# Kernel tuning notes

Measured on AMD Instinct MI355X. Metric: run time of the kernel, lower is better.

## Reference

```python
import jax, jax.numpy as jnp
import numpy as np

N_EMBD = 1024
HEAD_SIZE = 64  # n_embd // n_head = 1024 // 16


def setup_inputs() -> dict:
    key = jax.random.key(0)
    ks = jax.random.split(key, 7)
    B, T, C, H = 4, 2048, N_EMBD, HEAD_SIZE
    s = 1.0 / np.sqrt(C)
    return {
        "x": jax.random.normal(ks[0], (B, T, C), dtype=jnp.float32),
        "Wq": jax.random.normal(ks[1], (C, H), dtype=jnp.float32) * s,
        "bq": jax.random.normal(ks[2], (H,), dtype=jnp.float32) * 0.01,
        "Wk": jax.random.normal(ks[3], (C, H), dtype=jnp.float32) * s,
        "bk": jax.random.normal(ks[4], (H,), dtype=jnp.float32) * 0.01,
        "Wv": jax.random.normal(ks[5], (C, H), dtype=jnp.float32) * s,
        "bv": jax.random.normal(ks[6], (H,), dtype=jnp.float32) * 0.01,
    }


def reference(x, Wq, bq, Wk, bk, Wv, bv):
    # x: [B, T, C]
    B, T, C = x.shape
    q = x @ Wq + bq  # [B, T, H]
    k = x @ Wk + bk  # [B, T, H]
    v = x @ Wv + bv  # [B, T, H]
    # NOTE: original module does NOT scale by 1/sqrt(head_size)
    wei = jnp.einsum("bth,bsh->bts", q, k)  # [B, T, T]
    causal = jnp.tril(jnp.ones((T, T), dtype=bool))
    wei = jnp.where(causal, wei, -jnp.inf)
    wei = jax.nn.softmax(wei, axis=-1)
    out = jnp.einsum("bts,bsh->bth", wei, v)  # [B, T, H]
    return out
```

## Files before the change

kernel.cpp:

```cpp
#include <hip/hip_runtime.h>

typedef float f32x4 __attribute__((ext_vector_type(4)));
typedef short s16x4 __attribute__((ext_vector_type(4)));
typedef short s16x8 __attribute__((ext_vector_type(8)));

#define LOG2E 1.4426950408889634f

__device__ __forceinline__ short f2bf(float f) {
  unsigned u = __float_as_uint(f);
  unsigned r = (u + 0x7fffu + ((u >> 16) & 1u)) >> 16;
  return (short)r;
}
__device__ __forceinline__ float bf2f(short s) {
  return __uint_as_float(((unsigned)(unsigned short)s) << 16);
}
__device__ __forceinline__ unsigned cvt_pk_bf16(float a, float b) {
  unsigned r;
  asm("v_cvt_pk_bf16_f32 %0, %1, %2" : "=v"(r) : "v"(a), "v"(b));
  return r;
}

__device__ __forceinline__ f32x4 mfma16(s16x4 a, s16x4 b, f32x4 c) {
  return __builtin_amdgcn_mfma_f32_16x16x16bf16_1k(a, b, c, 0, 0, 0);
}
__device__ __forceinline__ f32x4 mfma32(s16x8 a, s16x8 b, f32x4 c) {
  return __builtin_amdgcn_mfma_f32_16x16x32_bf16(a, b, c, 0, 0, 0);
}

__device__ __forceinline__ void gl_lds16(const void* gp, void* sp) {
  __builtin_amdgcn_global_load_lds(
      (__attribute__((address_space(1))) void*)const_cast<void*>(gp),
      (__attribute__((address_space(3))) void*)sp, 16, 0, 0);
}

__global__ __launch_bounds__(256) void prep_w(
    const float* __restrict__ Wq, const float* __restrict__ Wk, const float* __restrict__ Wv,
    short* __restrict__ wt_hi, short* __restrict__ wt_lo) {
  int idx = blockIdx.x * 256 + threadIdx.x;
  int n = idx >> 10;
  int c = idx & 1023;
  const float* W = (n < 64) ? Wq : ((n < 128) ? Wk : Wv);
  float v = W[c * 64 + (n & 63)];
  short hi = f2bf(v);
  short lo = f2bf(v - bf2f(hi));
  wt_hi[idx] = hi;
  wt_lo[idx] = lo;
}

__global__ __launch_bounds__(512, 2) void proj_qkv(
    const float* __restrict__ x,
    const short* __restrict__ wt_hi, const short* __restrict__ wt_lo,
    const float* __restrict__ bq, const float* __restrict__ bk, const float* __restrict__ bv,
    short* __restrict__ q_hi, short* __restrict__ q_lo,
    short* __restrict__ k_hi, short* __restrict__ k_lo,
    short* __restrict__ v_t) {
  const int tid = threadIdx.x;
  const int lane = tid & 63;
  const int wv = tid >> 6;
  const int col = lane & 15;
  const int g = lane >> 4;
  const int mg = wv >> 2;
  const int ng = wv & 3;
  const int tokbase = blockIdx.x * 32;

  __shared__ short lds[5][12288];

  const int wsl = ((lane & 3) ^ ((lane >> 3) & 3)) * 8;
  const short* s0 = wt_hi + (size_t)(16 * wv + (lane >> 2)) * 1024 + wsl;
  const int d0 = wv * 512;
  const int c1 = wv + 8;
  const short* s1 = (c1 < 12 ? wt_hi + (size_t)(16 * c1 + (lane >> 2)) * 1024
                             : wt_lo + (size_t)(16 * (c1 - 12) + (lane >> 2)) * 1024) + wsl;
  const int d1 = (c1 < 12) ? c1 * 512 : 6144 + (c1 - 12) * 512;
  const int c2 = wv + 16;
  const bool isx = (c2 >= 20);
  const short* s2 = isx
      ? (const short*)(x + (size_t)(tokbase + 8 * (c2 - 20) + (lane >> 3)) * 1024 +
                       ((lane & 7) ^ (lane >> 3)) * 4)
      : wt_lo + (size_t)(16 * (c2 - 12) + (lane >> 2)) * 1024 + wsl;
  const int d2 = isx ? 10240 + (c2 - 20) * 512 : 6144 + (c2 - 12) * 512;
  const int st2 = isx ? 64 : 32;

#define STAGE(BP, S) do { \
    gl_lds16(s0 + (S) * 32, (BP) + d0); \
    gl_lds16(s1 + (S) * 32, (BP) + d1); \
    gl_lds16(s2 + (S) * st2, (BP) + d2); \
  } while (0)

#define PIPE_WAIT(N) do { \
    asm volatile("s_waitcnt vmcnt(" #N ")" ::: "memory"); \
    __builtin_amdgcn_s_barrier(); \
    __builtin_amdgcn_sched_barrier(0); \
  } while (0)
#define PIPE_END do { \
    asm volatile("s_waitcnt lgkmcnt(0)" ::: "memory"); \
    __builtin_amdgcn_sched_barrier(0); \
    __builtin_amdgcn_s_barrier(); \
  } while (0)

  const int arow = mg * 16 + col;
  const int xq0 = ((2 * g) ^ (arow & 7)) << 2;
  const int xq1 = ((2 * g + 1) ^ (arow & 7)) << 2;
  const int rq = ng * 16 + col;
  const int ws = (g ^ ((rq >> 1) & 3)) << 3;

  f32x4 accQ = {0,0,0,0}, accK = {0,0,0,0}, accV = {0,0,0,0};

  typedef union { unsigned u[4]; s16x8 v8; } pk8;

#define COMPUTE(BP) do { \
    const short* bp_ = (BP); \
    const float* xb_ = (const float*)(bp_ + 10240); \
    f32x4 x0_ = *(const f32x4*)(xb_ + arow * 32 + xq0); \
    f32x4 x1_ = *(const f32x4*)(xb_ + arow * 32 + xq1); \
    pk8 xh_, xl_; \
    xh_.u[0] = cvt_pk_bf16(x0_[0], x0_[1]); \
    xh_.u[1] = cvt_pk_bf16(x0_[2], x0_[3]); \
    xh_.u[2] = cvt_pk_bf16(x1_[0], x1_[1]); \
    xh_.u[3] = cvt_pk_bf16(x1_[2], x1_[3]); \
    xl_.u[0] = cvt_pk_bf16(x0_[0] - __uint_as_float(xh_.u[0] << 16), \
                           x0_[1] - __uint_as_float(xh_.u[0] & 0xffff0000u)); \
    xl_.u[1] = cvt_pk_bf16(x0_[2] - __uint_as_float(xh_.u[1] << 16), \
                           x0_[3] - __uint_as_float(xh_.u[1] & 0xffff0000u)); \
    xl_.u[2] = cvt_pk_bf16(x1_[0] - __uint_as_float(xh_.u[2] << 16), \
                           x1_[1] - __uint_as_float(xh_.u[2] & 0xffff0000u)); \
    xl_.u[3] = cvt_pk_bf16(x1_[2] - __uint_as_float(xh_.u[3] << 16), \
                           x1_[3] - __uint_as_float(xh_.u[3] & 0xffff0000u)); \
    s16x8 qh_ = *(const s16x8*)(bp_ + rq * 32 + ws); \
    s16x8 kh_ = *(const s16x8*)(bp_ + (64 + rq) * 32 + ws); \
    s16x8 vh_ = *(const s16x8*)(bp_ + (128 + rq) * 32 + ws); \
    s16x8 ql_ = *(const s16x8*)(bp_ + 6144 + rq * 32 + ws); \
    s16x8 kl_ = *(const s16x8*)(bp_ + 6144 + (64 + rq) * 32 + ws); \
    accQ = mfma32(xh_.v8, qh_, accQ); \
    accK = mfma32(xh_.v8, kh_, accK); \
    accV = mfma32(xh_.v8, vh_, accV); \
    accQ = mfma32(xl_.v8, qh_, accQ); \
    accK = mfma32(xl_.v8, kh_, accK); \
    accQ = mfma32(xh_.v8, ql_, accQ); \
    accK = mfma32(xh_.v8, kl_, accK); \
  } while (0)

  short* cA = &lds[0][0];
  short* cB = &lds[1][0];
  short* cC = &lds[2][0];
  short* cD = &lds[3][0];
  short* cE = &lds[4][0];

  STAGE(cA, 0); STAGE(cB, 1); STAGE(cC, 2); STAGE(cD, 3);

#pragma unroll 1
  for (int b = 0; b < 28; ++b) {
    STAGE(cE, b + 4);
    PIPE_WAIT(12);
    COMPUTE(cA);
    PIPE_END;
    short* t = cA; cA = cB; cB = cC; cC = cD; cD = cE; cE = t;
  }
  PIPE_WAIT(9); COMPUTE(cA); PIPE_END;
  PIPE_WAIT(6); COMPUTE(cB); PIPE_END;
  PIPE_WAIT(3); COMPUTE(cC); PIPE_END;
  PIPE_WAIT(0); COMPUTE(cD);

  {
    const int hQ = ng * 16 + col;
    const float biasq = bq[hQ];
    const float biask = bk[hQ];
    const float biasv = bv[hQ];
#pragma unroll
    for (int r = 0; r < 4; ++r) {
      const int tok = tokbase + mg * 16 + 4 * g + r;
      float fq = accQ[r] + biasq;
      short qh = f2bf(fq);
      q_hi[(size_t)tok * 64 + hQ] = qh;
      q_lo[(size_t)tok * 64 + hQ] = f2bf(fq - bf2f(qh));
      float fk = accK[r] + biask;
      short kh = f2bf(fk);
      k_hi[(size_t)tok * 64 + hQ] = kh;
      k_lo[(size_t)tok * 64 + hQ] = f2bf(fk - bf2f(kh));
      const int bb = tok >> 11;
      const int tl = tok & 2047;
      v_t[((size_t)bb * 64 + hQ) * 2048 + tl] = f2bf(accV[r] + biasv);
    }
  }
#undef STAGE
#undef PIPE_WAIT
#undef PIPE_END
#undef COMPUTE
}

__global__ __launch_bounds__(512, 2) void attn(
    const short* __restrict__ q_hi, const short* __restrict__ q_lo,
    const short* __restrict__ k_hi, const short* __restrict__ k_lo,
    const short* __restrict__ v_t,
    float* __restrict__ pm, float* __restrict__ pl, float* __restrict__ pO) {
  const int tid = threadIdx.x;
  const int lane = tid & 63;
  const int w = tid >> 6;
  const int col = lane & 15;
  const int g = lane >> 4;
  const int bid = blockIdx.x;
  const int p = bid & 7;
  const int b = (bid >> 3) & 3;
  const int s = bid >> 5;
  if (s > p) return;

  __shared__ short lds[3][12288];

  const int qlo = 256 * p + 32 * w;
  const int kb0 = 256 * s;

  const short* qbh = q_hi + (size_t)(b * 2048 + qlo + col) * 64 + g * 8;
  const short* qbl = q_lo + (size_t)(b * 2048 + qlo + col) * 64 + g * 8;
  s16x8 qh0a = *(const s16x8*)(qbh);
  s16x8 qh1a = *(const s16x8*)(qbh + 32);
  s16x8 ql0a = *(const s16x8*)(qbl);
  s16x8 ql1a = *(const s16x8*)(qbl + 32);
  s16x8 qh0b = *(const s16x8*)(qbh + 16 * 64);
  s16x8 qh1b = *(const s16x8*)(qbh + 16 * 64 + 32);
  s16x8 ql0b = *(const s16x8*)(qbl + 16 * 64);
  s16x8 ql1b = *(const s16x8*)(qbl + 16 * 64 + 32);
  asm volatile("s_waitcnt vmcnt(0)" ::: "memory");
  __builtin_amdgcn_sched_barrier(0);

  f32x4 oA0 = {0,0,0,0}, oA1 = {0,0,0,0}, oA2 = {0,0,0,0}, oA3 = {0,0,0,0};
  f32x4 oB0 = {0,0,0,0}, oB1 = {0,0,0,0}, oB2 = {0,0,0,0}, oB3 = {0,0,0,0};
  float mA = -3.0e38f, lA = 0.0f, mB = -3.0e38f, lB = 0.0f;
  const f32x4 NEGV = {-3.0e38f, -3.0e38f, -3.0e38f, -3.0e38f};

#define STAGE(BP, J) do { \
    const int kbs_ = kb0 + 64 * (J); \
    const int r_ = 8 * w + (lane >> 3); \
    const int lc_ = (lane & 7) ^ (lane >> 3); \
    gl_lds16(k_hi + (size_t)(b * 2048 + kbs_ + r_) * 64 + lc_ * 8, (BP) + 8 * w * 64); \
    gl_lds16(k_lo + (size_t)(b * 2048 + kbs_ + r_) * 64 + lc_ * 8, (BP) + 4096 + 8 * w * 64); \
    gl_lds16(v_t + ((size_t)b * 64 + r_) * 2048 + kbs_ + lc_ * 8, (BP) + 8192 + 8 * w * 64); \
  } while (0)

#define PIPE_WAIT(N) do { \
    asm volatile("s_waitcnt vmcnt(" #N ")" ::: "memory"); \
    __builtin_amdgcn_s_barrier(); \
    __builtin_amdgcn_sched_barrier(0); \
  } while (0)
#define PIPE_END do { \
    asm volatile("s_waitcnt lgkmcnt(0)" ::: "memory"); \
    __builtin_amdgcn_sched_barrier(0); \
    __builtin_amdgcn_s_barrier(); \
  } while (0)

#define QK_U(U) do { \
    const int kg0_ = kb_ + 16 * U; \
    if (kg0_ <= qlo + 31) { \
      const short* kr_ = bp_ + (16 * U + col) * 64; \
      const int cx_ = col & 7; \
      s16x8 kh0_ = *(const s16x8*)(kr_ + ((g ^ cx_) << 3)); \
      s16x8 kh1_ = *(const s16x8*)(kr_ + (((4 + g) ^ cx_) << 3)); \
      s16x8 kl0_ = *(const s16x8*)(kr_ + 4096 + ((g ^ cx_) << 3)); \
      s16x8 kl1_ = *(const s16x8*)(kr_ + 4096 + (((4 + g) ^ cx_) << 3)); \
      if (kg0_ <= qlo + 15) { \
        f32x4 u1_ = {0,0,0,0}, u2_ = {0,0,0,0}; \
        u1_ = mfma32(kh0_, qh0a, u1_); u1_ = mfma32(kh1_, qh1a, u1_); \
        u2_ = mfma32(kh0_, ql0a, u2_); u2_ = mfma32(kh1_, ql1a, u2_); \
        u2_ = mfma32(kl0_, qh0a, u2_); u2_ = mfma32(kl1_, qh1a, u2_); \
        scA##U = u1_ + u2_; \
        if (kg0_ == qlo) { \
          _Pragma("unroll") for (int i = 0; i < 4; ++i) \
            if (4 * g + i > col) scA##U[i] = -3.0e38f; \
        } \
      } \
      { \
        f32x4 u1_ = {0,0,0,0}, u2_ = {0,0,0,0}; \
        u1_ = mfma32(kh0_, qh0b, u1_); u1_ = mfma32(kh1_, qh1b, u1_); \
        u2_ = mfma32(kh0_, ql0b, u2_); u2_ = mfma32(kh1_, ql1b, u2_); \
        u2_ = mfma32(kl0_, qh0b, u2_); u2_ = mfma32(kl1_, qh1b, u2_); \
        scB##U = u1_ + u2_; \
        if (kg0_ == qlo + 16) { \
          _Pragma("unroll") for (int i = 0; i < 4; ++i) \
            if (4 * g + i > col) scB##U[i] = -3.0e38f; \
        } \
      } \
    } \
  } while (0)

#define SMAX4(v) fmaxf(fmaxf((v)[0], (v)[1]), fmaxf((v)[2], (v)[3]))

#define SOFTMAX_X(s0v, s1v, s2v, s3v, mX, lX, o0X, o1X, o2X, o3X, p0X, p1X, p2X, p3X) do { \
    float mx_ = fmaxf(fmaxf(SMAX4(s0v), SMAX4(s1v)), fmaxf(SMAX4(s2v), SMAX4(s3v))); \
    mx_ = fmaxf(mx_, __shfl_xor(mx_, 16)); \
    mx_ = fmaxf(mx_, __shfl_xor(mx_, 32)); \
    const float mn_ = fmaxf(mX, mx_); \
    const float rs_ = __builtin_amdgcn_exp2f((mX - mn_) * LOG2E); \
    float ls_ = 0.f; \
    _Pragma("unroll") for (int i = 0; i < 4; ++i) { \
      float e0_ = __builtin_amdgcn_exp2f((s0v[i] - mn_) * LOG2E); \
      float e1_ = __builtin_amdgcn_exp2f((s1v[i] - mn_) * LOG2E); \
      float e2_ = __builtin_amdgcn_exp2f((s2v[i] - mn_) * LOG2E); \
      float e3_ = __builtin_amdgcn_exp2f((s3v[i] - mn_) * LOG2E); \
      p0X[i] = f2bf(e0_); p1X[i] = f2bf(e1_); p2X[i] = f2bf(e2_); p3X[i] = f2bf(e3_); \
      ls_ += e0_ + e1_ + e2_ + e3_; \
    } \
    lX = lX * rs_ + ls_; \
    o0X *= rs_; o1X *= rs_; o2X *= rs_; o3X *= rs_; \
    mX = mn_; \
  } while (0)

#define PV_U(U) do { \
    const int kg0_ = kb_ + 16 * U; \
    if (kg0_ <= qlo + 31) { \
      const int cx_ = col & 7; \
      const short* vr_ = bp_ + 8192 + col * 64 + ((g & 1) << 2) + \
                         (((2 * U + (g >> 1)) ^ cx_) << 3); \
      s16x4 v0_ = *(const s16x4*)(vr_); \
      s16x4 v1_ = *(const s16x4*)(vr_ + 1024); \
      s16x4 v2_ = *(const s16x4*)(vr_ + 2048); \
      s16x4 v3_ = *(const s16x4*)(vr_ + 3072); \
      if (kg0_ <= qlo + 15) { \
        oA0 = mfma16(v0_, pbA##U, oA0); \
        oA1 = mfma16(v1_, pbA##U, oA1); \
        oA2 = mfma16(v2_, pbA##U, oA2); \
        oA3 = mfma16(v3_, pbA##U, oA3); \
      } \
      oB0 = mfma16(v0_, pbB##U, oB0); \
      oB1 = mfma16(v1_, pbB##U, oB1); \
      oB2 = mfma16(v2_, pbB##U, oB2); \
      oB3 = mfma16(v3_, pbB##U, oB3); \
    } \
  } while (0)

#define COMPUTE(BP, J) do { \
    const int kb_ = kb0 + 64 * (J); \
    if (kb_ <= qlo + 31) { \
      const short* bp_ = (BP); \
      f32x4 scA0 = NEGV, scA1 = NEGV, scA2 = NEGV, scA3 = NEGV; \
      f32x4 scB0 = NEGV, scB1 = NEGV, scB2 = NEGV, scB3 = NEGV; \
      QK_U(0); QK_U(1); QK_U(2); QK_U(3); \
      s16x4 pbA0, pbA1, pbA2, pbA3, pbB0, pbB1, pbB2, pbB3; \
      if (kb_ <= qlo + 15) \
        SOFTMAX_X(scA0, scA1, scA2, scA3, mA, lA, oA0, oA1, oA2, oA3, \
                  pbA0, pbA1, pbA2, pbA3); \
      SOFTMAX_X(scB0, scB1, scB2, scB3, mB, lB, oB0, oB1, oB2, oB3, \
                pbB0, pbB1, pbB2, pbB3); \
      PV_U(0); PV_U(1); PV_U(2); PV_U(3); \
    } \
  } while (0)

  short* L0 = &lds[0][0];
  short* L1 = &lds[1][0];
  short* L2 = &lds[2][0];

  STAGE(L0, 0); STAGE(L1, 1);
  STAGE(L2, 2); PIPE_WAIT(6); COMPUTE(L0, 0); PIPE_END;
  STAGE(L0, 3); PIPE_WAIT(6); COMPUTE(L1, 1); PIPE_END;
  PIPE_WAIT(3); COMPUTE(L2, 2); PIPE_END;
  PIPE_WAIT(0); COMPUTE(L0, 3);

  lA += __shfl_xor(lA, 16); lA += __shfl_xor(lA, 32);
  lB += __shfl_xor(lB, 16); lB += __shfl_xor(lB, 32);
  const int rowA = b * 2048 + qlo + col;
  const int rowB = rowA + 16;
  if (g == 0) {
    pm[s * 8192 + rowA] = mA;  pl[s * 8192 + rowA] = lA;
    pm[s * 8192 + rowB] = mB;  pl[s * 8192 + rowB] = lB;
  }
  {
    float* dA = pO + ((size_t)s * 8192 + rowA) * 64 + 4 * g;
    float* dB = pO + ((size_t)s * 8192 + rowB) * 64 + 4 * g;
    *(f32x4*)(dA)      = oA0; *(f32x4*)(dA + 16) = oA1;
    *(f32x4*)(dA + 32) = oA2; *(f32x4*)(dA + 48) = oA3;
    *(f32x4*)(dB)      = oB0; *(f32x4*)(dB + 16) = oB1;
    *(f32x4*)(dB + 32) = oB2; *(f32x4*)(dB + 48) = oB3;
  }
#undef STAGE
#undef PIPE_WAIT
#undef PIPE_END
#undef QK_U
#undef SMAX4
#undef SOFTMAX_X
#undef PV_U
#undef COMPUTE
}

__global__ __launch_bounds__(256) void reduce_p(
    const float* __restrict__ pm, const float* __restrict__ pl,
    const float* __restrict__ pO, float* __restrict__ out) {
  const int idx = blockIdx.x * 256 + threadIdx.x;
  const int row = idx >> 4;
  const int hq = (idx & 15) * 4;
  const int smax = (row & 2047) >> 8;
  float M = -3.0e38f;
  for (int s = 0; s <= smax; ++s) M = fmaxf(M, pm[s * 8192 + row]);
  float L = 0.f;
  f32x4 acc = {0, 0, 0, 0};
  for (int s = 0; s <= smax; ++s) {
    const float ws = __builtin_amdgcn_exp2f((pm[s * 8192 + row] - M) * LOG2E);
    L += ws * pl[s * 8192 + row];
    f32x4 ov = *(const f32x4*)(pO + ((size_t)s * 8192 + row) * 64 + hq);
    acc += ov * ws;
  }
  const float invL = 1.0f / L;
  *(f32x4*)(out + (size_t)row * 64 + hq) = acc * invL;
}

extern "C" void kernel_launch(void* const* d_in, const int* in_sizes, int n_in,
                              void* d_out, int out_size, void* d_ws, size_t ws_size,
                              hipStream_t stream) {
  const float* x  = (const float*)d_in[0];
  const float* Wq = (const float*)d_in[1];
  const float* bq = (const float*)d_in[2];
  const float* Wk = (const float*)d_in[3];
  const float* bk = (const float*)d_in[4];
  const float* Wv = (const float*)d_in[5];
  const float* bv = (const float*)d_in[6];
  float* out = (float*)d_out;

  char* ws = (char*)d_ws;
  short* wt_hi = (short*)(ws);
  short* wt_lo = (short*)(ws + 393216);
  short* q_hi  = (short*)(ws + 786432);
  short* q_lo  = (short*)(ws + 786432 + 1048576);
  short* k_hi  = (short*)(ws + 786432 + 2 * 1048576);
  short* k_lo  = (short*)(ws + 786432 + 3 * 1048576);
  short* v_t   = (short*)(ws + 786432 + 4 * 1048576);
  float* pm    = (float*)(ws + 6029312);
  float* pl    = (float*)(ws + 6291456);
  float* pO    = (float*)(ws + 6553600);

  hipLaunchKernelGGL(prep_w, dim3(768), dim3(256), 0, stream, Wq, Wk, Wv, wt_hi, wt_lo);
  hipLaunchKernelGGL(proj_qkv, dim3(256), dim3(512), 0, stream,
                     x, wt_hi, wt_lo, bq, bk, bv, q_hi, q_lo, k_hi, k_lo, v_t);
  hipLaunchKernelGGL(attn, dim3(256), dim3(512), 0, stream,
                     q_hi, q_lo, k_hi, k_lo, v_t, pm, pl, pO);
  hipLaunchKernelGGL(reduce_p, dim3(512), dim3(256), 0, stream, pm, pl, pO, out);
}
```

Baseline: 55.42 us.

## Process attention per 16-key subtile with lazy online-softmax rescaling

Restructures the inner loop so each 16-key subtile does QK, softmax and PV immediately instead of batching four subtiles of scores before softmax. Adds a lazy rescale: the running max and output rescale update only when some lane's new max exceeds the stored max by more than 8, which skips most exp/rescale work. This shrinks live score registers but serializes MFMA with softmax per subtile, which reduces instruction-level overlap. It also adds more cross-lane shuffles and wave votes per subtile. Unnormalized probabilities can reach up to e^8 before bf16 conversion, which is a small numerical risk.

```diff
diff --git a/kernel.cpp b/kernel.cpp
--- a/kernel.cpp
+++ b/kernel.cpp
@@ -225,7 +225,6 @@
   f32x4 oA0 = {0,0,0,0}, oA1 = {0,0,0,0}, oA2 = {0,0,0,0}, oA3 = {0,0,0,0};
   f32x4 oB0 = {0,0,0,0}, oB1 = {0,0,0,0}, oB2 = {0,0,0,0}, oB3 = {0,0,0,0};
   float mA = -3.0e38f, lA = 0.0f, mB = -3.0e38f, lB = 0.0f;
-  const f32x4 NEGV = {-3.0e38f, -3.0e38f, -3.0e38f, -3.0e38f};
 
 #define STAGE(BP, J) do { \
     const int kbs_ = kb0 + 64 * (J); \
@@ -247,82 +246,56 @@
     __builtin_amdgcn_s_barrier(); \
   } while (0)
 
-#define QK_U(U) do { \
+#define TILE_U(Qh0, Qh1, Ql0, Ql1, mX, lX, O0, O1, O2, O3, DIAG) do { \
+    f32x4 u1_ = {0,0,0,0}, u2_ = {0,0,0,0}; \
+    u1_ = mfma32(kh0_, Qh0, u1_); u1_ = mfma32(kh1_, Qh1, u1_); \
+    u2_ = mfma32(kh0_, Ql0, u2_); u2_ = mfma32(kh1_, Ql1, u2_); \
+    u2_ = mfma32(kl0_, Qh0, u2_); u2_ = mfma32(kl1_, Qh1, u2_); \
+    f32x4 s_ = u1_ + u2_; \
+    if (kg0_ == (DIAG)) { \
+      _Pragma("unroll") for (int i = 0; i < 4; ++i) \
+        if (4 * g + i > col) s_[i] = -3.0e38f; \
+    } \
+    float mx_ = fmaxf(fmaxf(s_[0], s_[1]), fmaxf(s_[2], s_[3])); \
+    mx_ = fmaxf(mx_, __shfl_xor(mx_, 16)); \
+    mx_ = fmaxf(mx_, __shfl_xor(mx_, 32)); \
+    if (!__all(mx_ <= mX + 8.0f)) { \
+      const float mn_ = fmaxf(mX, mx_); \
+      const float rs_ = __builtin_amdgcn_exp2f((mX - mn_) * LOG2E); \
+      lX *= rs_; O0 *= rs_; O1 *= rs_; O2 *= rs_; O3 *= rs_; \
+      mX = mn_; \
+    } \
+    const float p0_ = __builtin_amdgcn_exp2f((s_[0] - mX) * LOG2E); \
+    const float p1_ = __builtin_amdgcn_exp2f((s_[1] - mX) * LOG2E); \
+    const float p2_ = __builtin_amdgcn_exp2f((s_[2] - mX) * LOG2E); \
+    const float p3_ = __builtin_amdgcn_exp2f((s_[3] - mX) * LOG2E); \
+    lX += p0_ + p1_ + p2_ + p3_; \
+    s16x4 pb_; \
+    pb_[0] = f2bf(p0_); pb_[1] = f2bf(p1_); pb_[2] = f2bf(p2_); pb_[3] = f2bf(p3_); \
+    O0 = mfma16(v0_, pb_, O0); \
+    O1 = mfma16(v1_, pb_, O1); \
+    O2 = mfma16(v2_, pb_, O2); \
+    O3 = mfma16(v3_, pb_, O3); \
+  } while (0)
+
+#define STEP_U(U) do { \
     const int kg0_ = kb_ + 16 * U; \
     if (kg0_ <= qlo + 31) { \
+      const int cx_ = col & 7; \
       const short* kr_ = bp_ + (16 * U + col) * 64; \
-      const int cx_ = col & 7; \
       s16x8 kh0_ = *(const s16x8*)(kr_ + ((g ^ cx_) << 3)); \
       s16x8 kh1_ = *(const s16x8*)(kr_ + (((4 + g) ^ cx_) << 3)); \
       s16x8 kl0_ = *(const s16x8*)(kr_ + 4096 + ((g ^ cx_) << 3)); \
       s16x8 kl1_ = *(const s16x8*)(kr_ + 4096 + (((4 + g) ^ cx_) << 3)); \
-      if (kg0_ <= qlo + 15) { \
-        f32x4 u1_ = {0,0,0,0}, u2_ = {0,0,0,0}; \
-        u1_ = mfma32(kh0_, qh0a, u1_); u1_ = mfma32(kh1_, qh1a, u1_); \
-        u2_ = mfma32(kh0_, ql0a, u2_); u2_ = mfma32(kh1_, ql1a, u2_); \
-        u2_ = mfma32(kl0_, qh0a, u2_); u2_ = mfma32(kl1_, qh1a, u2_); \
-        scA##U = u1_ + u2_; \
-        if (kg0_ == qlo) { \
-          _Pragma("unroll") for (int i = 0; i < 4; ++i) \
-            if (4 * g + i > col) scA##U[i] = -3.0e38f; \
-        } \
-      } \
-      { \
-        f32x4 u1_ = {0,0,0,0}, u2_ = {0,0,0,0}; \
-        u1_ = mfma32(kh0_, qh0b, u1_); u1_ = mfma32(kh1_, qh1b, u1_); \
-        u2_ = mfma32(kh0_, ql0b, u2_); u2_ = mfma32(kh1_, ql1b, u2_); \
-        u2_ = mfma32(kl0_, qh0b, u2_); u2_ = mfma32(kl1_, qh1b, u2_); \
-        scB##U = u1_ + u2_; \
-        if (kg0_ == qlo + 16) { \
-          _Pragma("unroll") for (int i = 0; i < 4; ++i) \
-            if (4 * g + i > col) scB##U[i] = -3.0e38f; \
-        } \
-      } \
-    } \
-  } while (0)
-
-#define SMAX4(v) fmaxf(fmaxf((v)[0], (v)[1]), fmaxf((v)[2], (v)[3]))
-
-#define SOFTMAX_X(s0v, s1v, s2v, s3v, mX, lX, o0X, o1X, o2X, o3X, p0X, p1X, p2X, p3X) do { \
-    float mx_ = fmaxf(fmaxf(SMAX4(s0v), SMAX4(s1v)), fmaxf(SMAX4(s2v), SMAX4(s3v))); \
-    mx_ = fmaxf(mx_, __shfl_xor(mx_, 16)); \
-    mx_ = fmaxf(mx_, __shfl_xor(mx_, 32)); \
-    const float mn_ = fmaxf(mX, mx_); \
-    const float rs_ = __builtin_amdgcn_exp2f((mX - mn_) * LOG2E); \
-    float ls_ = 0.f; \
-    _Pragma("unroll") for (int i = 0; i < 4; ++i) { \
-      float e0_ = __builtin_amdgcn_exp2f((s0v[i] - mn_) * LOG2E); \
-      float e1_ = __builtin_amdgcn_exp2f((s1v[i] - mn_) * LOG2E); \
-      float e2_ = __builtin_amdgcn_exp2f((s2v[i] - mn_) * LOG2E); \
-      float e3_ = __builtin_amdgcn_exp2f((s3v[i] - mn_) * LOG2E); \
-      p0X[i] = f2bf(e0_); p1X[i] = f2bf(e1_); p2X[i] = f2bf(e2_); p3X[i] = f2bf(e3_); \
-      ls_ += e0_ + e1_ + e2_ + e3_; \
-    } \
-    lX = lX * rs_ + ls_; \
-    o0X *= rs_; o1X *= rs_; o2X *= rs_; o3X *= rs_; \
-    mX = mn_; \
-  } while (0)
-
-#define PV_U(U) do { \
-    const int kg0_ = kb_ + 16 * U; \
-    if (kg0_ <= qlo + 31) { \
-      const int cx_ = col & 7; \
       const short* vr_ = bp_ + 8192 + col * 64 + ((g & 1) << 2) + \
                          (((2 * U + (g >> 1)) ^ cx_) << 3); \
       s16x4 v0_ = *(const s16x4*)(vr_); \
       s16x4 v1_ = *(const s16x4*)(vr_ + 1024); \
       s16x4 v2_ = *(const s16x4*)(vr_ + 2048); \
       s16x4 v3_ = *(const s16x4*)(vr_ + 3072); \
-      if (kg0_ <= qlo + 15) { \
-        oA0 = mfma16(v0_, pbA##U, oA0); \
-        oA1 = mfma16(v1_, pbA##U, oA1); \
-        oA2 = mfma16(v2_, pbA##U, oA2); \
-        oA3 = mfma16(v3_, pbA##U, oA3); \
-      } \
-      oB0 = mfma16(v0_, pbB##U, oB0); \
-      oB1 = mfma16(v1_, pbB##U, oB1); \
-      oB2 = mfma16(v2_, pbB##U, oB2); \
-      oB3 = mfma16(v3_, pbB##U, oB3); \
+      TILE_U(qh0b, qh1b, ql0b, ql1b, mB, lB, oB0, oB1, oB2, oB3, qlo + 16); \
+      if (kg0_ <= qlo + 15) \
+        TILE_U(qh0a, qh1a, ql0a, ql1a, mA, lA, oA0, oA1, oA2, oA3, qlo); \
     } \
   } while (0)
 
@@ -330,16 +303,7 @@
     const int kb_ = kb0 + 64 * (J); \
     if (kb_ <= qlo + 31) { \
       const short* bp_ = (BP); \
-      f32x4 scA0 = NEGV, scA1 = NEGV, scA2 = NEGV, scA3 = NEGV; \
-      f32x4 scB0 = NEGV, scB1 = NEGV, scB2 = NEGV, scB3 = NEGV; \
-      QK_U(0); QK_U(1); QK_U(2); QK_U(3); \
-      s16x4 pbA0, pbA1, pbA2, pbA3, pbB0, pbB1, pbB2, pbB3; \
-      if (kb_ <= qlo + 15) \
-        SOFTMAX_X(scA0, scA1, scA2, scA3, mA, lA, oA0, oA1, oA2, oA3, \
-                  pbA0, pbA1, pbA2, pbA3); \
-      SOFTMAX_X(scB0, scB1, scB2, scB3, mB, lB, oB0, oB1, oB2, oB3, \
-                pbB0, pbB1, pbB2, pbB3); \
-      PV_U(0); PV_U(1); PV_U(2); PV_U(3); \
+      STEP_U(0); STEP_U(1); STEP_U(2); STEP_U(3); \
     } \
   } while (0)
 
@@ -372,10 +336,8 @@
 #undef STAGE
 #undef PIPE_WAIT
 #undef PIPE_END
-#undef QK_U
-#undef SMAX4
-#undef SOFTMAX_X
-#undef PV_U
+#undef TILE_U
+#undef STEP_U
 #undef COMPUTE
 }
 
```

Measured after the change: 56.72 us. 2.3% more time.
